# Optimization experiments

Hardware: AMD Instinct MI355X
Metric: run time of the kernel (lower is better)

## Reference

```python
import jax, jax.numpy as jnp
import numpy as np

H = 16
D = 1024
DH = D // H


def setup_inputs() -> dict:
    key = jax.random.key(0)
    ks = jax.random.split(key, 7)
    B, N = 4, 2048
    queries = jax.random.normal(ks[0], (B, N, D), dtype=jnp.float32)
    keys = jax.random.normal(ks[1], (B, N, D), dtype=jnp.float32)
    values = jax.random.normal(ks[2], (B, N, D), dtype=jnp.float32)
    s = 1.0 / np.sqrt(D)
    Wq = jax.random.normal(ks[3], (D, D), dtype=jnp.float32) * s
    Wk = jax.random.normal(ks[4], (D, D), dtype=jnp.float32) * s
    Wv = jax.random.normal(ks[5], (D, D), dtype=jnp.float32) * s
    Wo = jax.random.normal(ks[6], (D, D), dtype=jnp.float32) * s
    return {"queries": queries, "keys": keys, "values": values,
            "Wq": Wq, "Wk": Wk, "Wv": Wv, "Wo": Wo}


def reference(queries, keys, values, Wq, Wk, Wv, Wo):
    B, Nq, _ = queries.shape
    Nk = keys.shape[1]
    # torch Linear (no bias): y = x @ W.T
    q = (queries @ Wq.T).reshape(B, Nq, H, DH)
    k = (keys @ Wk.T).reshape(B, Nk, H, DH)
    v = (values @ Wv.T).reshape(B, Nk, H, DH)
    scale = 1.0 / jnp.sqrt(jnp.asarray(DH, dtype=q.dtype))
    scores = jnp.einsum("bqhd,bkhd->bhqk", q, k) * scale  # (B,H,Nq,Nk)
    attn = jax.nn.softmax(scores, axis=-1)
    ctx = jnp.einsum("bhqk,bkhd->bqhd", attn, v).reshape(B, Nq, D)
    return ctx @ Wo.T
```

## Files before the change

kernel.cpp:

```cpp
#include <hip/hip_runtime.h>
#include <hip/hip_bf16.h>
#include <stdint.h>

typedef short bf16x8 __attribute__((ext_vector_type(8)));
typedef float f32x4 __attribute__((ext_vector_type(4)));
typedef unsigned short u16;
typedef unsigned int u32;

#define MFMA(a, b, c) __builtin_amdgcn_mfma_f32_16x16x32_bf16(a, b, c, 0, 0, 0)

#if __has_builtin(__builtin_amdgcn_exp2f)
#define EXP2F(x) __builtin_amdgcn_exp2f(x)
#else
#define EXP2F(x) exp2f(x)
#endif
#if __has_builtin(__builtin_amdgcn_rcpf)
#define RCPF(x) __builtin_amdgcn_rcpf(x)
#else
#define RCPF(x) (1.0f / (x))
#endif

__device__ __forceinline__ u16 f2bf(float f) {
  return __builtin_bit_cast(u16, static_cast<__bf16>(f));
}

__device__ __forceinline__ bf16x8 cvt8(const float* p) {
  const float4 f0 = *(const float4*)p;
  const float4 f1 = *(const float4*)(p + 4);
  bf16x8 r;
  r[0] = (short)f2bf(f0.x); r[1] = (short)f2bf(f0.y);
  r[2] = (short)f2bf(f0.z); r[3] = (short)f2bf(f0.w);
  r[4] = (short)f2bf(f1.x); r[5] = (short)f2bf(f1.y);
  r[6] = (short)f2bf(f1.z); r[7] = (short)f2bf(f1.w);
  return r;
}

__device__ __forceinline__ void async16(const u16* g, u16* l) {
  __builtin_amdgcn_global_load_lds(
      (const __attribute__((address_space(1))) void*)g,
      (__attribute__((address_space(3))) void*)l, 16, 0, 0);
}

__global__ __launch_bounds__(256) void cvt_qk(const float* __restrict__ xq,
                                              const float* __restrict__ xk,
                                              u16* __restrict__ dq,
                                              u16* __restrict__ dk) {
  int b = (int)blockIdx.x;
  const float* s;
  u16* d;
  if (b < 4096) { s = xq; d = dq; } else { s = xk; d = dk; b -= 4096; }
  const size_t off = (size_t)b * 2048 + (size_t)threadIdx.x * 8;
  *(bf16x8*)(d + off) = cvt8(s + off);
}

__global__ __launch_bounds__(256) void cvt_vw(
    const float* __restrict__ xv, const float* __restrict__ wq,
    const float* __restrict__ wk, const float* __restrict__ wv,
    const float* __restrict__ wo, u16* __restrict__ dv, u16* __restrict__ dwq,
    u16* __restrict__ dwk, u16* __restrict__ dwv, u16* __restrict__ dwo) {
  int b = (int)blockIdx.x;
  const float* s;
  u16* d;
  if (b < 4096) { s = xv; d = dv; }
  else if (b < 4608) { s = wq; d = dwq; b -= 4096; }
  else if (b < 5120) { s = wk; d = dwk; b -= 4608; }
  else if (b < 5632) { s = wv; d = dwv; b -= 5120; }
  else { s = wo; d = dwo; b -= 5632; }
  const size_t off = (size_t)b * 2048 + (size_t)threadIdx.x * 8;
  *(bf16x8*)(d + off) = cvt8(s + off);
}

__device__ __forceinline__ void stage_gemm(const u16* __restrict__ A,
                                           const u16* __restrict__ W,
                                           u16* smA, u16* smB, int m0, int n0,
                                           int kk, int tid) {
  const int srow = tid >> 3, sblk = tid & 7;
#pragma unroll
  for (int jj = 0; jj < 4; ++jj) {
    const int row = jj * 32 + srow;
    const int sb = (sblk ^ (row & 7)) * 8;
    const int ld = (jj * 256 + tid) * 8;
    async16(A + (size_t)(m0 + row) * 1024 + kk * 64 + sb, smA + ld);
    async16(W + (size_t)(n0 + row) * 1024 + kk * 64 + sb, smB + ld);
  }
}

__device__ __forceinline__ void gemm_compute(const u16* smA, const u16* smB,
                                             f32x4 acc[4][4], int wm, int wn,
                                             int la, int q) {
#pragma unroll
  for (int ks = 0; ks < 2; ++ks) {
    bf16x8 af[4], bfr[4];
#pragma unroll
    for (int im = 0; im < 4; ++im)
      af[im] = *(const bf16x8*)(smA + (wm * 64 + im * 16 + la) * 64 +
                                (((ks * 4 + q) ^ (la & 7)) * 8));
#pragma unroll
    for (int in = 0; in < 4; ++in)
      bfr[in] = *(const bf16x8*)(smB + (wn * 64 + in * 16 + la) * 64 +
                                 (((ks * 4 + q) ^ (la & 7)) * 8));
#pragma unroll
    for (int im = 0; im < 4; ++im)
#pragma unroll
      for (int in = 0; in < 4; ++in)
        acc[im][in] = MFMA(af[im], bfr[in], acc[im][in]);
  }
}

__device__ __forceinline__ void gemm_core(const u16* __restrict__ A,
                                          const u16* __restrict__ W,
                                          u16* smA0, u16* smB0, u16* smA1,
                                          u16* smB1, f32x4 acc[4][4], int m0,
                                          int n0, int tid) {
  const int w = tid >> 6, l = tid & 63;
  const int la = l & 15, q = l >> 4;
  const int wm = w >> 1, wn = w & 1;

  stage_gemm(A, W, smA0, smB0, m0, n0, 0, tid);
  __syncthreads();
#pragma unroll 2
  for (int kk = 0; kk < 16; ++kk) {
    u16* ca = (kk & 1) ? smA1 : smA0;
    u16* cb = (kk & 1) ? smB1 : smB0;
    u16* na = (kk & 1) ? smA0 : smA1;
    u16* nb = (kk & 1) ? smB0 : smB1;
    if (kk < 15) stage_gemm(A, W, na, nb, m0, n0, kk + 1, tid);
    gemm_compute(ca, cb, acc, wm, wn, la, q);
    __syncthreads();
  }
}

__global__ __launch_bounds__(256, 2) void gemm_qkv(
    const u16* __restrict__ Xqb, const u16* __restrict__ Xkb,
    const u16* __restrict__ Xvb, const u16* __restrict__ Wqb,
    const u16* __restrict__ Wkb, const u16* __restrict__ Wvb,
    u16* __restrict__ Qh, u16* __restrict__ Kh, u16* __restrict__ VTp) {
  __shared__ u16 smA0[128 * 64], smB0[128 * 64];
  __shared__ u16 smA1[128 * 64], smB1[128 * 64];
  const int z = (int)blockIdx.z;
  const u16* A = (z == 0) ? Xqb : (z == 1) ? Xkb : Xvb;
  const u16* W = (z == 0) ? Wqb : (z == 1) ? Wkb : Wvb;
  u16* out = (z == 0) ? Qh : (z == 1) ? Kh : VTp;
  const float scale = (z == 0) ? 0.18033688011112042f : 1.0f;

  const int tid = (int)threadIdx.x;
  const int w = tid >> 6, l = tid & 63;
  const int la = l & 15, q = l >> 4;
  const int m0 = blockIdx.x * 128, n0 = blockIdx.y * 128;
  const int wm = w >> 1, wn = w & 1;

  f32x4 acc[4][4];
#pragma unroll
  for (int i = 0; i < 4; ++i)
#pragma unroll
    for (int j = 0; j < 4; ++j) acc[i][j] = (f32x4){0.f, 0.f, 0.f, 0.f};

  gemm_core(A, W, smA0, smB0, smA1, smB1, acc, m0, n0, tid);

#pragma unroll
  for (int im = 0; im < 4; ++im) {
    const int mbase = m0 + wm * 64 + im * 16 + q * 4;
#pragma unroll
    for (int in = 0; in < 4; ++in) {
      const int n = n0 + wn * 64 + in * 16 + la;
      if (z == 2) {
        const int b = mbase >> 11, nr = mbase & 2047;
        const int h = n >> 6, d = n & 63;
        uint2 val;
        val.x = (u32)f2bf(acc[im][in][0]) | ((u32)f2bf(acc[im][in][1]) << 16);
        val.y = (u32)f2bf(acc[im][in][2]) | ((u32)f2bf(acc[im][in][3]) << 16);
        *(uint2*)(VTp + ((size_t)((b * 16 + h) * 64 + d)) * 2048 + nr) = val;
      } else {
#pragma unroll
        for (int r = 0; r < 4; ++r) {
          const int mm = mbase + r;
          const int b = mm >> 11, nr = mm & 2047;
          const int h = n >> 6, d = n & 63;
          out[((size_t)((b * 16 + h) * 2048 + nr)) * 64 + d] =
              f2bf(acc[im][in][r] * scale);
        }
      }
    }
  }
}

__global__ __launch_bounds__(256, 2) void gemm_out(const u16* __restrict__ A,
                                                   const u16* __restrict__ W,
                                                   float* __restrict__ out) {
  __shared__ u16 smA0[128 * 64], smB0[128 * 64];
  __shared__ u16 smA1[128 * 64], smB1[128 * 64];
  const int tid = (int)threadIdx.x;
  const int w = tid >> 6, l = tid & 63;
  const int la = l & 15, q = l >> 4;
  const int m0 = blockIdx.x * 128, n0 = blockIdx.y * 128;
  const int wm = w >> 1, wn = w & 1;

  f32x4 acc[4][4];
#pragma unroll
  for (int i = 0; i < 4; ++i)
#pragma unroll
    for (int j = 0; j < 4; ++j) acc[i][j] = (f32x4){0.f, 0.f, 0.f, 0.f};

  gemm_core(A, W, smA0, smB0, smA1, smB1, acc, m0, n0, tid);

#pragma unroll
  for (int im = 0; im < 4; ++im) {
    const int mbase = m0 + wm * 64 + im * 16 + q * 4;
#pragma unroll
    for (int in = 0; in < 4; ++in) {
      const int n = n0 + wn * 64 + in * 16 + la;
#pragma unroll
      for (int r = 0; r < 4; ++r)
        out[(size_t)(mbase + r) * 1024 + n] = acc[im][in][r];
    }
  }
}

__global__ __launch_bounds__(256, 2) void attn_kernel(const u16* __restrict__ Qh,
                                                      const u16* __restrict__ Kh,
                                                      const u16* __restrict__ VT,
                                                      u16* __restrict__ ctx) {
  __shared__ u16 smK[128 * 64];
  __shared__ u16 smV0[64 * 128];
  __shared__ u16 smV1[64 * 128];
  __shared__ u16 smP[128 * 128];

  const int tid = (int)threadIdx.x;
  const int w = tid >> 6, l = tid & 63;
  const int la = l & 15, q = l >> 4;
  const int id = (int)blockIdx.x;
  const int slot = id >> 3;
  const int bh = (id & 7) * 8 + (slot >> 4);
  const int qt = slot & 15;
  const u16* Qp = Qh + (size_t)bh * (2048 * 64);
  const u16* Kp = Kh + (size_t)bh * (2048 * 64);
  const u16* Vp = VT + (size_t)bh * (64 * 2048);

  bf16x8 qf[2][2];
#pragma unroll
  for (int ic = 0; ic < 2; ++ic)
#pragma unroll
    for (int ks = 0; ks < 2; ++ks)
      qf[ic][ks] = *(const bf16x8*)(Qp + (size_t)(qt * 128 + w * 32 + ic * 16 + la) * 64 +
                                    ks * 32 + q * 8);

  f32x4 accO[2][4];
#pragma unroll
  for (int ic = 0; ic < 2; ++ic)
#pragma unroll
    for (int dc = 0; dc < 4; ++dc) accO[ic][dc] = (f32x4){0.f, 0.f, 0.f, 0.f};
  float m_[2] = {-__builtin_inff(), -__builtin_inff()};
  float l_[2] = {0.f, 0.f};
  float alpha_[2];
  bool skip_[2];

  const int srow = tid >> 3, sblk = tid & 7;

  auto stageK = [&](int kt_) {
#pragma unroll
    for (int jj = 0; jj < 4; ++jj) {
      const int krow = jj * 32 + srow;
      const int ksb = (sblk ^ (krow & 7)) * 8;
      async16(Kp + (size_t)(kt_ * 128 + krow) * 64 + ksb, smK + (jj * 256 + tid) * 8);
    }
  };
  auto stageV = [&](int kt_, u16* dst) {
#pragma unroll
    for (int jj = 0; jj < 4; ++jj) {
      const int idx = jj * 256 + tid;
      const int vr = idx >> 4, vb = idx & 15;
      async16(Vp + (size_t)vr * 2048 + kt_ * 128 + ((vb ^ (vr & 15)) * 8),
              dst + idx * 8);
    }
  };

  stageK(0);
  stageV(0, smV0);

  for (int kt = 0; kt < 16; ++kt) {
    u16* vcur = (kt & 1) ? smV1 : smV0;
    u16* vnxt = (kt & 1) ? smV0 : smV1;
    __syncthreads();

    f32x4 st[2][8];
#pragma unroll
    for (int ic = 0; ic < 2; ++ic)
#pragma unroll
      for (int jc = 0; jc < 8; ++jc) st[ic][jc] = (f32x4){0.f, 0.f, 0.f, 0.f};
    __builtin_amdgcn_s_setprio(1);
#pragma unroll
    for (int ks = 0; ks < 2; ++ks) {
      bf16x8 kf[8];
#pragma unroll
      for (int jc = 0; jc < 8; ++jc)
        kf[jc] = *(const bf16x8*)(smK + (jc * 16 + la) * 64 +
                                  (((ks * 4 + q) ^ (la & 7)) * 8));
#pragma unroll
      for (int jc = 0; jc < 8; ++jc)
#pragma unroll
        for (int ic = 0; ic < 2; ++ic)
          st[ic][jc] = MFMA(kf[jc], qf[ic][ks], st[ic][jc]);
    }
    __builtin_amdgcn_s_setprio(0);

#pragma unroll
    for (int ic = 0; ic < 2; ++ic) {
      float mx = -__builtin_inff();
#pragma unroll
      for (int jc = 0; jc < 8; ++jc)
#pragma unroll
        for (int r = 0; r < 4; ++r) mx = fmaxf(mx, st[ic][jc][r]);
      mx = fmaxf(mx, __shfl_xor(mx, 16));
      mx = fmaxf(mx, __shfl_xor(mx, 32));
      const bool skip = (bool)__all(mx - m_[ic] <= 8.0f);
      float mnew, al;
      if (skip) { mnew = m_[ic]; al = 1.0f; }
      else { mnew = fmaxf(m_[ic], mx); al = EXP2F(m_[ic] - mnew); }
      skip_[ic] = skip;
      alpha_[ic] = al;
      float rs = 0.f;
      const int i = w * 32 + ic * 16 + la;
#pragma unroll
      for (int jc = 0; jc < 8; ++jc) {
        const float p0 = EXP2F(st[ic][jc][0] - mnew);
        const float p1 = EXP2F(st[ic][jc][1] - mnew);
        const float p2 = EXP2F(st[ic][jc][2] - mnew);
        const float p3 = EXP2F(st[ic][jc][3] - mnew);
        rs += (p0 + p1) + (p2 + p3);
        uint2 val;
        val.x = (u32)f2bf(p0) | ((u32)f2bf(p1) << 16);
        val.y = (u32)f2bf(p2) | ((u32)f2bf(p3) << 16);
        const int blk = (jc * 2 + (q >> 1)) ^ la;
        *(uint2*)(smP + i * 128 + blk * 8 + (q & 1) * 4) = val;
      }
      rs += __shfl_xor(rs, 16);
      rs += __shfl_xor(rs, 32);
      m_[ic] = mnew;
      l_[ic] = l_[ic] * alpha_[ic] + rs;
    }
    __syncthreads();

    if (kt < 15) {
      stageK(kt + 1);
      stageV(kt + 1, vnxt);
    }

#pragma unroll
    for (int ic = 0; ic < 2; ++ic)
      if (!skip_[ic]) {
#pragma unroll
        for (int r = 0; r < 4; ++r) {
          const float a = __shfl(alpha_[ic], q * 4 + r);
#pragma unroll
          for (int dc = 0; dc < 4; ++dc) accO[ic][dc][r] *= a;
        }
      }

#pragma unroll
    for (int ks = 0; ks < 4; ++ks) {
      bf16x8 pf[2], vf[4];
#pragma unroll
      for (int ic = 0; ic < 2; ++ic)
        pf[ic] = *(const bf16x8*)(smP + (w * 32 + ic * 16 + la) * 128 +
                                  (((ks * 4 + q) ^ la) * 8));
#pragma unroll
      for (int dc = 0; dc < 4; ++dc)
        vf[dc] = *(const bf16x8*)(vcur + (dc * 16 + la) * 128 +
                                  (((ks * 4 + q) ^ la) * 8));
      __builtin_amdgcn_s_setprio(1);
#pragma unroll
      for (int ic = 0; ic < 2; ++ic)
#pragma unroll
        for (int dc = 0; dc < 4; ++dc)
          accO[ic][dc] = MFMA(pf[ic], vf[dc], accO[ic][dc]);
      __builtin_amdgcn_s_setprio(0);
    }
  }

  const int b = bh >> 4, h = bh & 15;
#pragma unroll
  for (int ic = 0; ic < 2; ++ic)
#pragma unroll
    for (int r = 0; r < 4; ++r) {
      const float inv = RCPF(__shfl(l_[ic], q * 4 + r));
      const size_t rowoff =
          ((size_t)(b * 2048 + qt * 128 + w * 32 + ic * 16 + q * 4 + r)) * 1024 + h * 64;
#pragma unroll
      for (int dc = 0; dc < 4; ++dc)
        ctx[rowoff + dc * 16 + la] = f2bf(accO[ic][dc][r] * inv);
    }
}

extern "C" void kernel_launch(void* const* d_in, const int* in_sizes, int n_in,
                              void* d_out, int out_size, void* d_ws, size_t ws_size,
                              hipStream_t stream) {
  const float* Xq = (const float*)d_in[0];
  const float* Xk = (const float*)d_in[1];
  const float* Xv = (const float*)d_in[2];
  const float* Wq = (const float*)d_in[3];
  const float* Wk = (const float*)d_in[4];
  const float* Wv = (const float*)d_in[5];
  const float* Wo = (const float*)d_in[6];

  const size_t T = 8388608;
  const size_t WN = 1048576;
  u16 *Xqb, *Xkb, *Xvb, *Wqb, *Wkb, *Wvb, *Wob, *Qh, *Kh, *VTp, *ctx;
  if (ws_size >= (7 * T + 4 * WN) * sizeof(u16)) {
    u16* ws = (u16*)d_ws;
    Xqb = ws; Xkb = ws + T; Xvb = ws + 2 * T;
    Qh = ws + 3 * T; Kh = ws + 4 * T; VTp = ws + 5 * T; ctx = ws + 6 * T;
    Wqb = ws + 7 * T; Wkb = Wqb + WN; Wvb = Wkb + WN; Wob = Wvb + WN;
  } else {
    u16* ob = (u16*)d_out;
    u16* bq = (u16*)d_in[0];
    u16* bk = (u16*)d_in[1];
    u16* bv = (u16*)d_in[2];
    Xqb = ob; Xkb = ob + T;
    Xvb = bq; Wqb = bq + T; Wkb = Wqb + WN; Wvb = Wkb + WN; Wob = Wvb + WN;
    Qh = bk; Kh = bk + T;
    VTp = bv; ctx = bv + T;
  }

  hipLaunchKernelGGL(cvt_qk, dim3(8192), dim3(256), 0, stream, Xq, Xk, Xqb, Xkb);
  hipLaunchKernelGGL(cvt_vw, dim3(6144), dim3(256), 0, stream, Xv, Wq, Wk, Wv, Wo,
                     Xvb, Wqb, Wkb, Wvb, Wob);
  hipLaunchKernelGGL(gemm_qkv, dim3(64, 8, 3), dim3(256), 0, stream, Xqb, Xkb, Xvb,
                     Wqb, Wkb, Wvb, Qh, Kh, VTp);
  hipLaunchKernelGGL(attn_kernel, dim3(1024), dim3(256), 0, stream, Qh, Kh, VTp, ctx);
  hipLaunchKernelGGL(gemm_out, dim3(64, 8), dim3(256), 0, stream, ctx, Wob, (float*)d_out);
}
```

Measured before the change: 327.4 us.

## Compute softmax row sums via MFMA and vectorize GEMM epilogue stores

The attention kernel drops the per-row VALU summation and shuffle reductions of the softmax denominator. Instead it adds an extra MFMA per tile that multiplies P by a ones vector, so the row sum is taken from the bf16-rounded P (a slight numeric change). The Q/K projections and the output GEMM swap MFMA operand order so each lane holds contiguous output columns. This lets the epilogues write 8-byte bf16 packs or float4 instead of scalar stores. The max reduction is also restructured into 3-input max chains.

```diff
diff --git a/kernel.cpp b/kernel.cpp
--- a/kernel.cpp
+++ b/kernel.cpp
@@ -85,6 +85,7 @@
   }
 }
 
+template <bool SWAP>
 __device__ __forceinline__ void gemm_compute(const u16* smA, const u16* smB,
                                              f32x4 acc[4][4], int wm, int wn,
                                              int la, int q) {
@@ -102,11 +103,16 @@
 #pragma unroll
     for (int im = 0; im < 4; ++im)
 #pragma unroll
-      for (int in = 0; in < 4; ++in)
-        acc[im][in] = MFMA(af[im], bfr[in], acc[im][in]);
-  }
-}
-
+      for (int in = 0; in < 4; ++in) {
+        if (SWAP)
+          acc[in][im] = MFMA(bfr[in], af[im], acc[in][im]);
+        else
+          acc[im][in] = MFMA(af[im], bfr[in], acc[im][in]);
+      }
+  }
+}
+
+template <bool SWAP>
 __device__ __forceinline__ void gemm_core(const u16* __restrict__ A,
                                           const u16* __restrict__ W,
                                           u16* smA0, u16* smB0, u16* smA1,
@@ -125,7 +131,7 @@
     u16* na = (kk & 1) ? smA0 : smA1;
     u16* nb = (kk & 1) ? smB0 : smB1;
     if (kk < 15) stage_gemm(A, W, na, nb, m0, n0, kk + 1, tid);
-    gemm_compute(ca, cb, acc, wm, wn, la, q);
+    gemm_compute<SWAP>(ca, cb, acc, wm, wn, la, q);
     __syncthreads();
   }
 }
@@ -155,30 +161,37 @@
 #pragma unroll
     for (int j = 0; j < 4; ++j) acc[i][j] = (f32x4){0.f, 0.f, 0.f, 0.f};
 
-  gemm_core(A, W, smA0, smB0, smA1, smB1, acc, m0, n0, tid);
-
-#pragma unroll
-  for (int im = 0; im < 4; ++im) {
-    const int mbase = m0 + wm * 64 + im * 16 + q * 4;
-#pragma unroll
-    for (int in = 0; in < 4; ++in) {
-      const int n = n0 + wn * 64 + in * 16 + la;
-      if (z == 2) {
+  if (z == 2) {
+    gemm_core<false>(A, W, smA0, smB0, smA1, smB1, acc, m0, n0, tid);
+#pragma unroll
+    for (int im = 0; im < 4; ++im) {
+      const int mbase = m0 + wm * 64 + im * 16 + q * 4;
+#pragma unroll
+      for (int in = 0; in < 4; ++in) {
+        const int n = n0 + wn * 64 + in * 16 + la;
         const int b = mbase >> 11, nr = mbase & 2047;
         const int h = n >> 6, d = n & 63;
         uint2 val;
         val.x = (u32)f2bf(acc[im][in][0]) | ((u32)f2bf(acc[im][in][1]) << 16);
         val.y = (u32)f2bf(acc[im][in][2]) | ((u32)f2bf(acc[im][in][3]) << 16);
         *(uint2*)(VTp + ((size_t)((b * 16 + h) * 64 + d)) * 2048 + nr) = val;
-      } else {
-#pragma unroll
-        for (int r = 0; r < 4; ++r) {
-          const int mm = mbase + r;
-          const int b = mm >> 11, nr = mm & 2047;
-          const int h = n >> 6, d = n & 63;
-          out[((size_t)((b * 16 + h) * 2048 + nr)) * 64 + d] =
-              f2bf(acc[im][in][r] * scale);
-        }
+      }
+    }
+  } else {
+    gemm_core<true>(A, W, smA0, smB0, smA1, smB1, acc, m0, n0, tid);
+#pragma unroll
+    for (int in = 0; in < 4; ++in) {
+      const int nbase = n0 + wn * 64 + in * 16 + q * 4;
+      const int h = nbase >> 6, dd = nbase & 63;
+#pragma unroll
+      for (int im = 0; im < 4; ++im) {
+        const int m = m0 + wm * 64 + im * 16 + la;
+        const int b = m >> 11, nr = m & 2047;
+        const f32x4 a = acc[in][im];
+        uint2 val;
+        val.x = (u32)f2bf(a[0] * scale) | ((u32)f2bf(a[1] * scale) << 16);
+        val.y = (u32)f2bf(a[2] * scale) | ((u32)f2bf(a[3] * scale) << 16);
+        *(uint2*)(out + ((size_t)((b * 16 + h) * 2048 + nr)) * 64 + dd) = val;
       }
     }
   }
@@ -201,17 +214,17 @@
 #pragma unroll
     for (int j = 0; j < 4; ++j) acc[i][j] = (f32x4){0.f, 0.f, 0.f, 0.f};
 
-  gemm_core(A, W, smA0, smB0, smA1, smB1, acc, m0, n0, tid);
-
-#pragma unroll
-  for (int im = 0; im < 4; ++im) {
-    const int mbase = m0 + wm * 64 + im * 16 + q * 4;
-#pragma unroll
-    for (int in = 0; in < 4; ++in) {
-      const int n = n0 + wn * 64 + in * 16 + la;
-#pragma unroll
-      for (int r = 0; r < 4; ++r)
-        out[(size_t)(mbase + r) * 1024 + n] = acc[im][in][r];
+  gemm_core<true>(A, W, smA0, smB0, smA1, smB1, acc, m0, n0, tid);
+
+#pragma unroll
+  for (int in = 0; in < 4; ++in) {
+    const int nbase = n0 + wn * 64 + in * 16 + q * 4;
+#pragma unroll
+    for (int im = 0; im < 4; ++im) {
+      const int m = m0 + wm * 64 + im * 16 + la;
+      const f32x4 a = acc[in][im];
+      *(float4*)(out + (size_t)m * 1024 + nbase) =
+          make_float4(a[0], a[1], a[2], a[3]);
     }
   }
 }
@@ -244,13 +257,16 @@
       qf[ic][ks] = *(const bf16x8*)(Qp + (size_t)(qt * 128 + w * 32 + ic * 16 + la) * 64 +
                                     ks * 32 + q * 8);
 
-  f32x4 accO[2][4];
+  bf16x8 onesf;
+#pragma unroll
+  for (int j = 0; j < 8; ++j) onesf[j] = (short)0x3F80;
+
+  f32x4 accO[2][5];
 #pragma unroll
   for (int ic = 0; ic < 2; ++ic)
 #pragma unroll
-    for (int dc = 0; dc < 4; ++dc) accO[ic][dc] = (f32x4){0.f, 0.f, 0.f, 0.f};
+    for (int dc = 0; dc < 5; ++dc) accO[ic][dc] = (f32x4){0.f, 0.f, 0.f, 0.f};
   float m_[2] = {-__builtin_inff(), -__builtin_inff()};
-  float l_[2] = {0.f, 0.f};
   float alpha_[2];
   bool skip_[2];
 
@@ -307,9 +323,10 @@
     for (int ic = 0; ic < 2; ++ic) {
       float mx = -__builtin_inff();
 #pragma unroll
-      for (int jc = 0; jc < 8; ++jc)
-#pragma unroll
-        for (int r = 0; r < 4; ++r) mx = fmaxf(mx, st[ic][jc][r]);
+      for (int jc = 0; jc < 8; ++jc) {
+        const float t0 = fmaxf(fmaxf(st[ic][jc][0], st[ic][jc][1]), st[ic][jc][2]);
+        mx = fmaxf(fmaxf(mx, t0), st[ic][jc][3]);
+      }
       mx = fmaxf(mx, __shfl_xor(mx, 16));
       mx = fmaxf(mx, __shfl_xor(mx, 32));
       const bool skip = (bool)__all(mx - m_[ic] <= 8.0f);
@@ -318,7 +335,6 @@
       else { mnew = fmaxf(m_[ic], mx); al = EXP2F(m_[ic] - mnew); }
       skip_[ic] = skip;
       alpha_[ic] = al;
-      float rs = 0.f;
       const int i = w * 32 + ic * 16 + la;
 #pragma unroll
       for (int jc = 0; jc < 8; ++jc) {
@@ -326,17 +342,13 @@
         const float p1 = EXP2F(st[ic][jc][1] - mnew);
         const float p2 = EXP2F(st[ic][jc][2] - mnew);
         const float p3 = EXP2F(st[ic][jc][3] - mnew);
-        rs += (p0 + p1) + (p2 + p3);
         uint2 val;
         val.x = (u32)f2bf(p0) | ((u32)f2bf(p1) << 16);
         val.y = (u32)f2bf(p2) | ((u32)f2bf(p3) << 16);
         const int blk = (jc * 2 + (q >> 1)) ^ la;
         *(uint2*)(smP + i * 128 + blk * 8 + (q & 1) * 4) = val;
       }
-      rs += __shfl_xor(rs, 16);
-      rs += __shfl_xor(rs, 32);
       m_[ic] = mnew;
-      l_[ic] = l_[ic] * alpha_[ic] + rs;
     }
     __syncthreads();
 
@@ -352,7 +364,7 @@
         for (int r = 0; r < 4; ++r) {
           const float a = __shfl(alpha_[ic], q * 4 + r);
 #pragma unroll
-          for (int dc = 0; dc < 4; ++dc) accO[ic][dc][r] *= a;
+          for (int dc = 0; dc < 5; ++dc) accO[ic][dc][r] *= a;
         }
       }
 
@@ -369,10 +381,12 @@
                                   (((ks * 4 + q) ^ la) * 8));
       __builtin_amdgcn_s_setprio(1);
 #pragma unroll
-      for (int ic = 0; ic < 2; ++ic)
+      for (int ic = 0; ic < 2; ++ic) {
 #pragma unroll
         for (int dc = 0; dc < 4; ++dc)
           accO[ic][dc] = MFMA(pf[ic], vf[dc], accO[ic][dc]);
+        accO[ic][4] = MFMA(pf[ic], onesf, accO[ic][4]);
+      }
       __builtin_amdgcn_s_setprio(0);
     }
   }
@@ -382,7 +396,7 @@
   for (int ic = 0; ic < 2; ++ic)
 #pragma unroll
     for (int r = 0; r < 4; ++r) {
-      const float inv = RCPF(__shfl(l_[ic], q * 4 + r));
+      const float inv = RCPF(accO[ic][4][r]);
       const size_t rowoff =
           ((size_t)(b * 2048 + qt * 128 + w * 32 + ic * 16 + q * 4 + r)) * 1024 + h * 64;
 #pragma unroll
```

New measurement: 345.0 us. 5.4% more time.
